# Optimization experiments

Hardware: AMD Instinct MI355X
Metric: run time of the kernel (lower is better)

The kernel has to match this reference:

```python
import jax, jax.numpy as jnp
import numpy as np

AC, H = 32, 8          # attention_num_c, num_heads
C1, C2 = 256, 128      # rep_1d num_c, rep_2d num_c
B, NR, NA, M = 1, 512, 256, 8
EPS = 1e-5


def _ln(x, g, b):
    mu = jnp.mean(x, axis=-1, keepdims=True)
    var = jnp.mean(jnp.square(x - mu), axis=-1, keepdims=True)
    return (x - mu) * jax.lax.rsqrt(var + EPS) * g + b


def setup_inputs() -> dict:
    key = jax.random.key(0)
    ks = jax.random.split(key, 16)
    s = 0.02
    return {
        "rec_profile": jax.random.normal(ks[0], (B, NR, C1), jnp.float32),
        "lig_profile": jax.random.normal(ks[1], (B, M, NA, C1), jnp.float32),
        "pair": jax.random.normal(ks[2], (B, NR + NA, NR + NA, C2), jnp.float32),
        "rec_norm_g": jnp.ones((C1,), jnp.float32),
        "rec_norm_b": jnp.zeros((C1,), jnp.float32),
        "lig_norm_g": jnp.ones((C1,), jnp.float32),
        "lig_norm_b": jnp.zeros((C1,), jnp.float32),
        "W_rec_qkv": jax.random.normal(ks[3], (C1, 6 * AC * H), jnp.float32) * s,
        "W_lig_qkv": jax.random.normal(ks[4], (C1, 6 * AC * H), jnp.float32) * s,
        "W_rr": jax.random.normal(ks[5], (C2, H), jnp.float32) * s,
        "W_ll": jax.random.normal(ks[6], (C2, H), jnp.float32) * s,
        "W_rl": jax.random.normal(ks[7], (C2, H), jnp.float32) * s,
        "W_lr": jax.random.normal(ks[8], (C2, H), jnp.float32) * s,
        "W_rec_fin": jax.random.normal(ks[9], (AC * H, C1), jnp.float32) * s,
        "b_rec_fin": jnp.zeros((C1,), jnp.float32),
        "W_lig_fin": jax.random.normal(ks[10], (AC * H, C1), jnp.float32) * s,
        "b_lig_fin": jnp.zeros((C1,), jnp.float32),
    }


def reference(rec_profile, lig_profile, pair, rec_norm_g, rec_norm_b,
              lig_norm_g, lig_norm_b, W_rec_qkv, W_lig_qkv,
              W_rr, W_ll, W_rl, W_lr,
              W_rec_fin, b_rec_fin, W_lig_fin, b_lig_fin):
    nr = rec_profile.shape[1]
    m = lig_profile.shape[1]
    na = lig_profile.shape[2]

    rec = _ln(rec_profile, rec_norm_g, rec_norm_b)           # [b,nr,C1]
    lig = _ln(lig_profile, lig_norm_g, lig_norm_b)           # [b,m,na,C1]

    rqkv = (rec @ W_rec_qkv).reshape(*rec.shape[:-1], AC, 6 * H)
    rec_lq, rec_lk, rec_lv, rec_rq, rec_rk, rec_rv = jnp.split(rqkv, 6, axis=-1)
    lqkv = (lig @ W_lig_qkv).reshape(*lig.shape[:-1], AC, 6 * H)
    lig_lq, lig_lk, lig_lv, lig_rq, lig_rk, lig_rv = jnp.split(lqkv, 6, axis=-1)

    # affinities (note: original does NOT scale the qk products, only the pair biases)
    rr_aff = jnp.einsum('bich,bjch->bijh', rec_rq, rec_rk)          # [b,nr,nr,h]
    rl_aff = jnp.einsum('bich,bmjch->bmijh', rec_lq, lig_rk)        # [b,m,nr,na,h]
    lr_aff = jnp.einsum('bich,bmjch->bmjih', rec_lk, lig_rq)        # [b,m,na,nr,h]
    ll_aff = jnp.einsum('bmich,bmjch->bmijh', lig_lq, lig_lk)       # [b,m,na,na,h]

    factor = 1.0 / np.sqrt(AC).astype(np.float32)
    rr_b = (pair[:, :nr, :nr] @ W_rr) * factor                      # [b,nr,nr,h]
    rl_b = (pair[:, :nr, nr:] @ W_rl) * factor                      # [b,nr,na,h]
    lr_b = (pair[:, nr:, :nr] @ W_lr) * factor                      # [b,na,nr,h]
    ll_b = (pair[:, nr:, nr:] @ W_ll) * factor                      # [b,na,na,h]

    top_left = jnp.broadcast_to((rr_aff + rr_b)[:, None],
                                (rr_aff.shape[0], m, nr, nr, H))
    top = jnp.concatenate([top_left, rl_aff + rl_b[:, None]], axis=3)   # [b,m,nr,N,h]
    bot = jnp.concatenate([lr_aff + lr_b[:, None], ll_aff + ll_b[:, None]], axis=3)  # [b,m,na,N,h]
    w = jnp.concatenate([top, bot], axis=2)                              # [b,m,N,N,h]
    w = jax.nn.softmax(w, axis=3)  # softmax over dim=-2 (keys j)

    rec_out = (jnp.einsum('brch,birh->bich', rec_rv, w[:, 0, :nr, :nr]) +
               jnp.einsum('bmrch,bmirh->bmich', lig_rv, w[:, :, :nr, nr:]).mean(1))
    lig_out = (jnp.einsum('bmrch,bmirh->bmich', lig_lv, w[:, :, nr:, nr:]) +
               jnp.einsum('brch,bmirh->bmich', rec_lv, w[:, :, nr:, :nr]))

    rec_out = rec_out.reshape(*rec_out.shape[:-2], -1) @ W_rec_fin + b_rec_fin
    lig_out = lig_out.reshape(*lig_out.shape[:-2], -1) @ W_lig_fin + b_lig_fin
    return rec_out, lig_out
```

## Files before the change

kernel.cpp:

```cpp
#include <hip/hip_runtime.h>
#include <hip/hip_bf16.h>

#define AC 32
#define H 8
#define C1 256
#define C2 128
#define NR 512
#define NA 256
#define MM 8
#define NN 768
#define QKVD 1536
#define F 256


__global__ __launch_bounds__(256) void ln_kernel(
    const float* __restrict__ in, const float* __restrict__ g,
    const float* __restrict__ b, float* __restrict__ xn, int nrows)
{
    const int t = threadIdx.x, w = t >> 6, lane = t & 63;
    const int row = blockIdx.x * 4 + w;
    if (row >= nrows) return;
    const float4 v = ((const float4*)(in + (size_t)row * C1))[lane];
    float s  = v.x + v.y + v.z + v.w;
    float s2 = v.x * v.x + v.y * v.y + v.z * v.z + v.w * v.w;
    #pragma unroll
    for (int off = 32; off; off >>= 1) {
        s  += __shfl_xor(s, off);
        s2 += __shfl_xor(s2, off);
    }
    const float mu = s * (1.0f / C1);
    const float rs = rsqrtf(s2 * (1.0f / C1) - mu * mu + 1e-5f);
    const float4 gv = ((const float4*)g)[lane];
    const float4 bv = ((const float4*)b)[lane];
    float4 o;
    o.x = (v.x - mu) * rs * gv.x + bv.x;
    o.y = (v.y - mu) * rs * gv.y + bv.y;
    o.z = (v.z - mu) * rs * gv.z + bv.z;
    o.w = (v.w - mu) * rs * gv.w + bv.w;
    ((float4*)(xn + (size_t)row * C1))[lane] = o;
}

__global__ __launch_bounds__(256) void qkv_gemm(
    const float* __restrict__ xn, const float* __restrict__ W,
    float* __restrict__ out, int nrows)
{
    __shared__ float x[4][C1];
    const int t = threadIdx.x;
    const int base = blockIdx.x * 4;
    #pragma unroll
    for (int r = 0; r < 4; ++r) x[r][t] = xn[(size_t)(base + r) * C1 + t];
    __syncthreads();

    const int col  = blockIdx.y * 256 + t;
    const int c    = col / 48;
    const int rem  = col - c * 48;
    const int role = rem >> 3;
    const int h    = rem & 7;
    const int f    = c * 8 + h;

    float a0 = 0.f, a1 = 0.f, a2 = 0.f, a3 = 0.f;
    #pragma unroll 4
    for (int cc = 0; cc < C1; ++cc) {
        const float w = W[(size_t)cc * QKVD + col];
        a0 += x[0][cc] * w;
        a1 += x[1][cc] * w;
        a2 += x[2][cc] * w;
        a3 += x[3][cc] * w;
    }
    float* op = out + ((size_t)role * nrows + base) * F + f;
    op[0 * F] = a0; op[1 * F] = a1; op[2 * F] = a2; op[3 * F] = a3;
}

__global__ __launch_bounds__(256) void pair_bias_kernel(
    const float* __restrict__ pair, const float* __restrict__ Wrr,
    const float* __restrict__ Wll, const float* __restrict__ Wrl,
    const float* __restrict__ Wlr, float* __restrict__ bias)
{
    const int t = threadIdx.x;
    const int grp = t >> 5, l = t & 31;
    const int q = blockIdx.y;
    const int kbase = blockIdx.x * 32;

    const float* W;
    if (q < NR) W = (kbase < NR) ? Wrr : Wrl;
    else        W = (kbase < NR) ? Wlr : Wll;

    const float factor = 0.17677669529663687f;

    float wreg[4][8];
    #pragma unroll
    for (int i = 0; i < 4; ++i) {
        const float4 a  = *(const float4*)(W + (size_t)(l * 4 + i) * H);
        const float4 b4 = *(const float4*)(W + (size_t)(l * 4 + i) * H + 4);
        wreg[i][0] = a.x * factor;  wreg[i][1] = a.y * factor;
        wreg[i][2] = a.z * factor;  wreg[i][3] = a.w * factor;
        wreg[i][4] = b4.x * factor; wreg[i][5] = b4.y * factor;
        wreg[i][6] = b4.z * factor; wreg[i][7] = b4.w * factor;
    }

    const int hsel = 4 * (l & 1) + 2 * ((l >> 1) & 1) + ((l >> 2) & 1);

    #pragma unroll
    for (int kk = 0; kk < 4; ++kk) {
        const int k = kbase + kk * 8 + grp;

        const float4 p = *(const float4*)(pair + ((size_t)q * NN + k) * C2 + l * 4);
        float pr[4] = {p.x, p.y, p.z, p.w};

        float acc[8];
        #pragma unroll
        for (int h = 0; h < 8; ++h)
            acc[h] = pr[0] * wreg[0][h] + pr[1] * wreg[1][h] +
                     pr[2] * wreg[2][h] + pr[3] * wreg[3][h];

        {
            const bool b = (l & 1) != 0;
            float s0 = b ? acc[0] : acc[4];
            float s1 = b ? acc[1] : acc[5];
            float s2 = b ? acc[2] : acc[6];
            float s3 = b ? acc[3] : acc[7];
            const float r0 = __shfl_xor(s0, 1);
            const float r1 = __shfl_xor(s1, 1);
            const float r2 = __shfl_xor(s2, 1);
            const float r3 = __shfl_xor(s3, 1);
            acc[0] = (b ? acc[4] : acc[0]) + r0;
            acc[1] = (b ? acc[5] : acc[1]) + r1;
            acc[2] = (b ? acc[6] : acc[2]) + r2;
            acc[3] = (b ? acc[7] : acc[3]) + r3;
        }
        {
            const bool b = (l & 2) != 0;
            float s0 = b ? acc[0] : acc[2];
            float s1 = b ? acc[1] : acc[3];
            const float r0 = __shfl_xor(s0, 2);
            const float r1 = __shfl_xor(s1, 2);
            acc[0] = (b ? acc[2] : acc[0]) + r0;
            acc[1] = (b ? acc[3] : acc[1]) + r1;
        }
        float v;
        {
            const bool b = (l & 4) != 0;
            float s0 = b ? acc[0] : acc[1];
            const float r0 = __shfl_xor(s0, 4);
            v = (b ? acc[1] : acc[0]) + r0;
        }
        v += __shfl_xor(v, 8);
        v += __shfl_xor(v, 16);

        if (l < 8)
            bias[((size_t)q * NN + k) * H + hsel] = v;
    }
}

__global__ __launch_bounds__(256) void rr_add_kernel(
    const float* __restrict__ rqkv, float* __restrict__ bias)
{
    __shared__ __align__(16) float qv[F];
    const int t = threadIdx.x;
    const int q = blockIdx.x;
    const size_t RSTR = (size_t)NR * F;
    qv[t] = rqkv[3 * RSTR + (size_t)q * F + t];
    __syncthreads();
    const float4* q4 = (const float4*)qv;
    const float* recK = rqkv + 4 * RSTR;

    #pragma unroll
    for (int rep = 0; rep < 2; ++rep) {
        const int k = rep * 256 + t;
        const float4* krow = (const float4*)(recK + (size_t)k * F);
        float acc[8] = {0.f, 0.f, 0.f, 0.f, 0.f, 0.f, 0.f, 0.f};
        #pragma unroll 8
        for (int j = 0; j < 64; ++j) {
            const float4 kv = krow[j];
            const float4 qq = q4[j];
            const int hb = (j & 1) * 4;
            acc[hb + 0] += qq.x * kv.x;
            acc[hb + 1] += qq.y * kv.y;
            acc[hb + 2] += qq.z * kv.z;
            acc[hb + 3] += qq.w * kv.w;
        }
        float* bp = bias + ((size_t)q * NN + k) * H;
        const float4 b1 = ((const float4*)bp)[0];
        const float4 b2 = ((const float4*)bp)[1];
        ((float4*)bp)[0] = make_float4(acc[0] + b1.x, acc[1] + b1.y,
                                       acc[2] + b1.z, acc[3] + b1.w);
        ((float4*)bp)[1] = make_float4(acc[4] + b2.x, acc[5] + b2.y,
                                       acc[6] + b2.z, acc[7] + b2.w);
    }
}

__global__ __launch_bounds__(256) void attn_kernel(
    const float* __restrict__ rqkv, const float* __restrict__ lqkv,
    const float* __restrict__ bias, float* __restrict__ rec_att,
    float* __restrict__ lig_att)
{
    __shared__ __align__(16) float qA[2][F];
    __shared__ __align__(16) float qB[2][F];
    __shared__ float ptile[2][256][9];
    __shared__ float red2[2][32][8];
    __shared__ float Mrun[2][8], Drun[2][8], fct[2][8];

    const int t = threadIdx.x;
    const int q0 = blockIdx.x * 2, m = blockIdx.y;
    const bool top = q0 < NR;

    const size_t RSTR = (size_t)NR * F;
    const size_t LSTR = (size_t)MM * NA * F;
    const float* recP = rqkv;
    const float* ligP = lqkv + (size_t)m * NA * F;

    #pragma unroll
    for (int r = 0; r < 2; ++r) {
        const float* qrow = top ? (recP + (size_t)(q0 + r) * F)
                                : (ligP + (size_t)(q0 + r - NR) * F);
        const size_t str = top ? RSTR : LSTR;
        qA[r][t] = qrow[3 * str + t];
        qB[r][t] = qrow[0 * str + t];
    }
    if (t < 16) { Mrun[t >> 3][t & 7] = -1e30f; Drun[t >> 3][t & 7] = 0.f; }
    __syncthreads();

    const float* recK = recP + (top ? 4 : 1) * RSTR;
    const float* ligK = ligP + (top ? 4 : 1) * LSTR;
    const float* Vrec = recP + (top ? 5 : 2) * RSTR;
    const float* Vlig = ligP + (top ? 5 : 2) * LSTR;

    const int h = t & 7, s = t >> 3;
    float accR0 = 0.f, accR1 = 0.f, accL0 = 0.f, accL1 = 0.f;

    for (int tl = 0; tl < 3; ++tl) {
        const int kbase = tl * 256;
        if (top && tl < 2) {
            #pragma unroll
            for (int r = 0; r < 2; ++r) {
                const float* bp = bias + ((size_t)(q0 + r) * NN + kbase + t) * H;
                const float4 b1 = ((const float4*)bp)[0];
                const float4 b2 = ((const float4*)bp)[1];
                ptile[r][t][0] = b1.x; ptile[r][t][1] = b1.y;
                ptile[r][t][2] = b1.z; ptile[r][t][3] = b1.w;
                ptile[r][t][4] = b2.x; ptile[r][t][5] = b2.y;
                ptile[r][t][6] = b2.z; ptile[r][t][7] = b2.w;
            }
        } else {
            const float4* krow = (const float4*)((tl < 2)
                ? (recK + (size_t)(kbase + t) * F)
                : (ligK + (size_t)t * F));
            float acc[2][8] = {{0.f}};
            #pragma unroll 8
            for (int j = 0; j < 64; ++j) {
                const float4 kv = krow[j];
                const int hb = (j & 1) * 4;
                #pragma unroll
                for (int r = 0; r < 2; ++r) {
                    const float4 qq = (tl < 2) ? ((const float4*)qA[r])[j]
                                               : ((const float4*)qB[r])[j];
                    acc[r][hb + 0] += qq.x * kv.x;
                    acc[r][hb + 1] += qq.y * kv.y;
                    acc[r][hb + 2] += qq.z * kv.z;
                    acc[r][hb + 3] += qq.w * kv.w;
                }
            }
            #pragma unroll
            for (int r = 0; r < 2; ++r) {
                const float* bp = bias + ((size_t)(q0 + r) * NN + kbase + t) * H;
                const float4 b1 = ((const float4*)bp)[0];
                const float4 b2 = ((const float4*)bp)[1];
                ptile[r][t][0] = acc[r][0] + b1.x; ptile[r][t][1] = acc[r][1] + b1.y;
                ptile[r][t][2] = acc[r][2] + b1.z; ptile[r][t][3] = acc[r][3] + b1.w;
                ptile[r][t][4] = acc[r][4] + b2.x; ptile[r][t][5] = acc[r][5] + b2.y;
                ptile[r][t][6] = acc[r][6] + b2.z; ptile[r][t][7] = acc[r][7] + b2.w;
            }
        }
        __syncthreads();

        #pragma unroll
        for (int r = 0; r < 2; ++r) {
            float pm = ptile[r][s * 8][h];
            #pragma unroll
            for (int j = 1; j < 8; ++j) pm = fmaxf(pm, ptile[r][s * 8 + j][h]);
            red2[r][s][h] = pm;
        }
        __syncthreads();
        if (t < 16) {
            const int r = t >> 3, hh = t & 7;
            float mx = red2[r][0][hh];
            for (int s2 = 1; s2 < 32; ++s2) mx = fmaxf(mx, red2[r][s2][hh]);
            const float Mo = Mrun[r][hh];
            const float Mn = fmaxf(Mo, mx);
            fct[r][hh]  = __expf(Mo - Mn);
            Mrun[r][hh] = Mn;
        }
        __syncthreads();

        #pragma unroll
        for (int r = 0; r < 2; ++r) {
            const float Mn = Mrun[r][h];
            float ps = 0.f;
            #pragma unroll
            for (int j = 0; j < 8; ++j) {
                const int kk = s * 8 + j;
                const float e = __expf(ptile[r][kk][h] - Mn);
                ptile[r][kk][h] = e;
                ps += e;
            }
            red2[r][s][h] = ps;
        }
        {
            const float f0 = fct[0][h], f1 = fct[1][h];
            accR0 *= f0; accL0 *= f0;
            accR1 *= f1; accL1 *= f1;
        }
        __syncthreads();
        if (t < 16) {
            const int r = t >> 3, hh = t & 7;
            float ts = 0.f;
            for (int s2 = 0; s2 < 32; ++s2) ts += red2[r][s2][hh];
            Drun[r][hh] = Drun[r][hh] * fct[r][hh] + ts;
        }

        const bool doPV = (tl == 2) || (!top) || (m == 0);
        if (doPV) {
            if (tl < 2) {
                const float* Vp = Vrec + (size_t)kbase * F;
                #pragma unroll 8
                for (int kk = 0; kk < 256; ++kk) {
                    const float v = Vp[(size_t)kk * F + t];
                    accR0 += ptile[0][kk][h] * v;
                    accR1 += ptile[1][kk][h] * v;
                }
            } else {
                #pragma unroll 8
                for (int kk = 0; kk < 256; ++kk) {
                    const float v = Vlig[(size_t)kk * F + t];
                    accL0 += ptile[0][kk][h] * v;
                    accL1 += ptile[1][kk][h] * v;
                }
            }
        }
        __syncthreads();
    }

    const float i0 = 1.0f / Drun[0][h];
    const float i1 = 1.0f / Drun[1][h];
    if (top) {
        atomicAdd(&rec_att[(size_t)q0 * F + t],       i0 * (accR0 + 0.125f * accL0));
        atomicAdd(&rec_att[(size_t)(q0 + 1) * F + t], i1 * (accR1 + 0.125f * accL1));
    } else {
        const int i = q0 - NR;
        lig_att[((size_t)m * NA + i) * F + t]     = i0 * (accR0 + accL0);
        lig_att[((size_t)m * NA + i + 1) * F + t] = i1 * (accR1 + accL1);
    }
}

__global__ __launch_bounds__(256) void final_gemm(
    const float* __restrict__ att, const float* __restrict__ W,
    const float* __restrict__ bfin, float* __restrict__ out, int nrows)
{
    __shared__ float x[4][C1];
    const int t = threadIdx.x;
    const int base = blockIdx.x * 4;
    #pragma unroll
    for (int r = 0; r < 4; ++r) x[r][t] = att[(size_t)(base + r) * C1 + t];
    __syncthreads();
    float a0 = 0.f, a1 = 0.f, a2 = 0.f, a3 = 0.f;
    #pragma unroll 4
    for (int cc = 0; cc < C1; ++cc) {
        const float w = W[(size_t)cc * C1 + t];
        a0 += x[0][cc] * w;
        a1 += x[1][cc] * w;
        a2 += x[2][cc] * w;
        a3 += x[3][cc] * w;
    }
    const float bb = bfin[t];
    out[(size_t)(base + 0) * C1 + t] = a0 + bb;
    out[(size_t)(base + 1) * C1 + t] = a1 + bb;
    out[(size_t)(base + 2) * C1 + t] = a2 + bb;
    out[(size_t)(base + 3) * C1 + t] = a3 + bb;
}

extern "C" void kernel_launch(void* const* d_in, const int* in_sizes, int n_in,
                              void* d_out, int out_size, void* d_ws, size_t ws_size,
                              hipStream_t stream) {
    const float* rec_profile = (const float*)d_in[0];
    const float* lig_profile = (const float*)d_in[1];
    const float* pair        = (const float*)d_in[2];
    const float* rec_g       = (const float*)d_in[3];
    const float* rec_b       = (const float*)d_in[4];
    const float* lig_g       = (const float*)d_in[5];
    const float* lig_b       = (const float*)d_in[6];
    const float* W_rec_qkv   = (const float*)d_in[7];
    const float* W_lig_qkv   = (const float*)d_in[8];
    const float* W_rr        = (const float*)d_in[9];
    const float* W_ll        = (const float*)d_in[10];
    const float* W_rl        = (const float*)d_in[11];
    const float* W_lr        = (const float*)d_in[12];
    const float* W_rec_fin   = (const float*)d_in[13];
    const float* b_rec_fin   = (const float*)d_in[14];
    const float* W_lig_fin   = (const float*)d_in[15];
    const float* b_lig_fin   = (const float*)d_in[16];

    float* ws      = (float*)d_ws;
    float* rqkv    = ws;
    float* lqkv    = rqkv + (size_t)NR * QKVD;
    float* bias    = lqkv + (size_t)MM * NA * QKVD;
    float* rec_att = bias + (size_t)NN * NN * H;
    float* lig_att = rec_att + (size_t)NR * F;

    float* xn_rec = rec_att;
    float* xn_lig = lig_att;

    ln_kernel<<<NR / 4, 256, 0, stream>>>(rec_profile, rec_g, rec_b, xn_rec, NR);
    ln_kernel<<<MM * NA / 4, 256, 0, stream>>>(lig_profile, lig_g, lig_b,
                                               xn_lig, MM * NA);
    qkv_gemm<<<dim3(NR / 4, 6), 256, 0, stream>>>(xn_rec, W_rec_qkv, rqkv, NR);
    qkv_gemm<<<dim3(MM * NA / 4, 6), 256, 0, stream>>>(xn_lig, W_lig_qkv,
                                                       lqkv, MM * NA);
    pair_bias_kernel<<<dim3(NN / 32, NN), 256, 0, stream>>>(pair, W_rr, W_ll,
                                                            W_rl, W_lr, bias);
    rr_add_kernel<<<NR, 256, 0, stream>>>(rqkv, bias);

    hipMemsetAsync(rec_att, 0, (size_t)NR * F * sizeof(float), stream);

    attn_kernel<<<dim3(NN / 2, MM), 256, 0, stream>>>(rqkv, lqkv, bias,
                                                      rec_att, lig_att);

    float* rec_out = (float*)d_out;
    float* lig_out = rec_out + (size_t)NR * C1;
    final_gemm<<<NR / 4, 256, 0, stream>>>(rec_att, W_rec_fin, b_rec_fin,
                                           rec_out, NR);
    final_gemm<<<MM * NA / 4, 256, 0, stream>>>(lig_att, W_lig_fin, b_lig_fin,
                                                lig_out, MM * NA);
}
```

Before: 869.8 us.

## Split PV accumulation across key groups with float4 V loads and LDS reduction

The PV loop in the attention kernel now has each thread own 4 consecutive channels and a quarter of the keys (64 of 256), loading V as float4 instead of scalar. This cuts the serial loop length per thread and widens global loads. The four key-group partial sums are reduced through shared memory (reusing ptile) after the loop, at the cost of an extra sync and LDS traffic. ptile reads of 4 heads per key may hit bank conflicts because of the row stride of 9.

```diff
diff --git a/kernel.cpp b/kernel.cpp
--- a/kernel.cpp
+++ b/kernel.cpp
@@ -196,9 +196,9 @@
 {
     __shared__ __align__(16) float qA[2][F];
     __shared__ __align__(16) float qB[2][F];
-    __shared__ float ptile[2][256][9];
+    __shared__ __align__(16) float ptile[2][256][9];
     __shared__ float red2[2][32][8];
-    __shared__ float Mrun[2][8], Drun[2][8], fct[2][8];
+    __shared__ __align__(16) float Mrun[2][8], Drun[2][8], fct[2][8];
 
     const int t = threadIdx.x;
     const int q0 = blockIdx.x * 2, m = blockIdx.y;
@@ -226,7 +226,12 @@
     const float* Vlig = ligP + (top ? 5 : 2) * LSTR;
 
     const int h = t & 7, s = t >> 3;
-    float accR0 = 0.f, accR1 = 0.f, accL0 = 0.f, accL1 = 0.f;
+    const int g_pv = t >> 6;
+    const int u_pv = t & 63;
+    const int hb4 = 4 * (t & 1);
+
+    float aR[2][4] = {{0.f, 0.f, 0.f, 0.f}, {0.f, 0.f, 0.f, 0.f}};
+    float aL[2][4] = {{0.f, 0.f, 0.f, 0.f}, {0.f, 0.f, 0.f, 0.f}};
 
     for (int tl = 0; tl < 3; ++tl) {
         const int kbase = tl * 256;
@@ -306,9 +311,12 @@
             red2[r][s][h] = ps;
         }
         {
-            const float f0 = fct[0][h], f1 = fct[1][h];
-            accR0 *= f0; accL0 *= f0;
-            accR1 *= f1; accL1 *= f1;
+            const float4 f0 = *(const float4*)&fct[0][hb4];
+            const float4 f1 = *(const float4*)&fct[1][hb4];
+            aR[0][0] *= f0.x; aR[0][1] *= f0.y; aR[0][2] *= f0.z; aR[0][3] *= f0.w;
+            aL[0][0] *= f0.x; aL[0][1] *= f0.y; aL[0][2] *= f0.z; aL[0][3] *= f0.w;
+            aR[1][0] *= f1.x; aR[1][1] *= f1.y; aR[1][2] *= f1.z; aR[1][3] *= f1.w;
+            aL[1][0] *= f1.x; aL[1][1] *= f1.y; aL[1][2] *= f1.z; aL[1][3] *= f1.w;
         }
         __syncthreads();
         if (t < 16) {
@@ -323,32 +331,62 @@
             if (tl < 2) {
                 const float* Vp = Vrec + (size_t)kbase * F;
                 #pragma unroll 8
-                for (int kk = 0; kk < 256; ++kk) {
-                    const float v = Vp[(size_t)kk * F + t];
-                    accR0 += ptile[0][kk][h] * v;
-                    accR1 += ptile[1][kk][h] * v;
+                for (int kk2 = 0; kk2 < 64; ++kk2) {
+                    const int kk = g_pv * 64 + kk2;
+                    const float4 v4 = *(const float4*)(Vp + (size_t)kk * F + 4 * u_pv);
+                    #pragma unroll
+                    for (int r = 0; r < 2; ++r) {
+                        aR[r][0] += ptile[r][kk][hb4 + 0] * v4.x;
+                        aR[r][1] += ptile[r][kk][hb4 + 1] * v4.y;
+                        aR[r][2] += ptile[r][kk][hb4 + 2] * v4.z;
+                        aR[r][3] += ptile[r][kk][hb4 + 3] * v4.w;
+                    }
                 }
             } else {
                 #pragma unroll 8
-                for (int kk = 0; kk < 256; ++kk) {
-                    const float v = Vlig[(size_t)kk * F + t];
-                    accL0 += ptile[0][kk][h] * v;
-                    accL1 += ptile[1][kk][h] * v;
+                for (int kk2 = 0; kk2 < 64; ++kk2) {
+                    const int kk = g_pv * 64 + kk2;
+                    const float4 v4 = *(const float4*)(Vlig + (size_t)kk * F + 4 * u_pv);
+                    #pragma unroll
+                    for (int r = 0; r < 2; ++r) {
+                        aL[r][0] += ptile[r][kk][hb4 + 0] * v4.x;
+                        aL[r][1] += ptile[r][kk][hb4 + 1] * v4.y;
+                        aL[r][2] += ptile[r][kk][hb4 + 2] * v4.z;
+                        aL[r][3] += ptile[r][kk][hb4 + 3] * v4.w;
+                    }
                 }
             }
         }
         __syncthreads();
+    }
+
+    float* redf = &ptile[0][0][0];
+    #pragma unroll
+    for (int r = 0; r < 2; ++r) {
+        *(float4*)(redf + ((g_pv * 2 + r) * 2 + 0) * 256 + 4 * u_pv) =
+            make_float4(aR[r][0], aR[r][1], aR[r][2], aR[r][3]);
+        *(float4*)(redf + ((g_pv * 2 + r) * 2 + 1) * 256 + 4 * u_pv) =
+            make_float4(aL[r][0], aL[r][1], aL[r][2], aL[r][3]);
+    }
+    __syncthreads();
+    float R0 = 0.f, L0 = 0.f, R1 = 0.f, L1 = 0.f;
+    #pragma unroll
+    for (int g2 = 0; g2 < 4; ++g2) {
+        R0 += redf[((g2 * 2 + 0) * 2 + 0) * 256 + t];
+        L0 += redf[((g2 * 2 + 0) * 2 + 1) * 256 + t];
+        R1 += redf[((g2 * 2 + 1) * 2 + 0) * 256 + t];
+        L1 += redf[((g2 * 2 + 1) * 2 + 1) * 256 + t];
     }
 
     const float i0 = 1.0f / Drun[0][h];
     const float i1 = 1.0f / Drun[1][h];
     if (top) {
-        atomicAdd(&rec_att[(size_t)q0 * F + t],       i0 * (accR0 + 0.125f * accL0));
-        atomicAdd(&rec_att[(size_t)(q0 + 1) * F + t], i1 * (accR1 + 0.125f * accL1));
+        atomicAdd(&rec_att[(size_t)q0 * F + t],       i0 * (R0 + 0.125f * L0));
+        atomicAdd(&rec_att[(size_t)(q0 + 1) * F + t], i1 * (R1 + 0.125f * L1));
     } else {
         const int i = q0 - NR;
-        lig_att[((size_t)m * NA + i) * F + t]     = i0 * (accR0 + accL0);
-        lig_att[((size_t)m * NA + i + 1) * F + t] = i1 * (accR1 + accL1);
+        lig_att[((size_t)m * NA + i) * F + t]     = i0 * (R0 + L0);
+        lig_att[((size_t)m * NA + i + 1) * F + t] = i1 * (R1 + L1);
     }
 }
 
```

Measured after the change: 868.5 us. About the same (-0.2%).
